# Performance work log

Hardware: AMD Instinct MI355X
Metric: run time of the kernel (lower is better)

Reference implementation:

```python
import jax, jax.numpy as jnp
import numpy as np

B, S, D = 2, 2048, 2048
H = 16
HD = D // H

def setup_inputs() -> dict:
    key = jax.random.key(0)
    ks = jax.random.split(key, 6)
    s = 1.0 / np.sqrt(D)
    return {
        "inputs": jax.random.normal(ks[0], (B, S, D), dtype=jnp.float32),
        "w_q": jax.random.normal(ks[1], (D, D), dtype=jnp.float32) * s,
        "w_k": jax.random.normal(ks[2], (D, D), dtype=jnp.float32) * s,
        "w_v": jax.random.normal(ks[3], (D, D), dtype=jnp.float32) * s,
        "w_o": jax.random.normal(ks[4], (D, D), dtype=jnp.float32) * s,
        "b_o": jax.random.normal(ks[5], (D,), dtype=jnp.float32) * 0.02,
    }

def reference(inputs, w_q, w_k, w_v, w_o, b_o):
    b, t, _ = inputs.shape
    # Linear layers: y = x @ W^T (weights stored torch-style [out, in])
    q = (inputs @ w_q.T).reshape(b, t, H, HD)
    k = (inputs @ w_k.T).reshape(b, t, H, HD)
    v = (inputs @ w_v.T).reshape(b, t, H, HD)
    # scores: [b, h, t, t]
    scores = jnp.einsum('bqhd,bkhd->bhqk', q, k)
    causal = jnp.triu(jnp.ones((t, t), dtype=bool), k=1)
    scores = jnp.where(causal, -jnp.inf, scores)
    # NOTE: source scales by sqrt(token_num) (keys.shape[2] after transpose), not sqrt(head_dim)
    scale = jnp.float32(t) ** 0.5
    attn = jax.nn.softmax(scores / scale, axis=-1)
    ctx = jnp.einsum('bhqk,bkhd->bqhd', attn, v).reshape(b, t, D)
    return ctx @ w_o.T + b_o
```

## Files before the change

kernel.cpp:

```cpp
#include <hip/hip_runtime.h>


typedef __attribute__((ext_vector_type(8))) short short8;
typedef __attribute__((ext_vector_type(4))) float f32x4;

#define SEQ 2048
#define DM  2048
#define NHD 128
#define QSCALE (0.022097086912079608f * 1.4426950408889634f)

#define EXP2F(x) __builtin_amdgcn_exp2f(x)

__device__ __forceinline__ unsigned short f2bf(float f) {
  unsigned u = __builtin_bit_cast(unsigned, f);
  u += 0x7FFFu + ((u >> 16) & 1u);
  return (unsigned short)(u >> 16);
}

__device__ __forceinline__ void gll16(const void* g, void* l) {
  __builtin_amdgcn_global_load_lds((const __attribute__((address_space(1))) void*)g,
                                   (__attribute__((address_space(3))) void*)l, 16, 0, 0);
}

template <int CTRL>
__device__ __forceinline__ float dpp_mv(float x) {
  int xi = __builtin_bit_cast(int, x);
  return __builtin_bit_cast(float,
      __builtin_amdgcn_update_dpp(xi, xi, CTRL, 0xF, 0xF, false));
}
__device__ __forceinline__ float red16_max(float x) {
  x = fmaxf(x, dpp_mv<0xB1>(x));
  x = fmaxf(x, dpp_mv<0x4E>(x));
  x = fmaxf(x, dpp_mv<0x124>(x));
  x = fmaxf(x, dpp_mv<0x128>(x));
  return x;
}
__device__ __forceinline__ float red16_sum(float x) {
  x += dpp_mv<0xB1>(x);
  x += dpp_mv<0x4E>(x);
  x += dpp_mv<0x124>(x);
  x += dpp_mv<0x128>(x);
  return x;
}

__global__ __launch_bounds__(256) void cast_bf16_k(const float* __restrict__ in,
                                                   unsigned short* __restrict__ out,
                                                   int n8) {
  int i = blockIdx.x * 256 + threadIdx.x;
  if (i >= n8) return;
  const f32x4* p = (const f32x4*)in + (size_t)i * 2;
  f32x4 a = p[0], b = p[1];
  short8 o;
  o[0] = (short)f2bf(a[0]); o[1] = (short)f2bf(a[1]);
  o[2] = (short)f2bf(a[2]); o[3] = (short)f2bf(a[3]);
  o[4] = (short)f2bf(b[0]); o[5] = (short)f2bf(b[1]);
  o[6] = (short)f2bf(b[2]); o[7] = (short)f2bf(b[3]);
  *(short8*)(out + (size_t)i * 8) = o;
}

__global__ __launch_bounds__(256) void cast_w4_k(const float* __restrict__ Wq,
                                                 const float* __restrict__ Wk,
                                                 const float* __restrict__ Wv,
                                                 const float* __restrict__ Wo,
                                                 unsigned short* __restrict__ Wqb,
                                                 unsigned short* __restrict__ Wkb,
                                                 unsigned short* __restrict__ Wvb,
                                                 unsigned short* __restrict__ Wob) {
  int i = blockIdx.x * 256 + threadIdx.x;
  int r = i >> 19, j = i & 524287;
  const float* src = (r == 0) ? Wq : (r == 1) ? Wk : (r == 2) ? Wv : Wo;
  unsigned short* dst = (r == 0) ? Wqb : (r == 1) ? Wkb : (r == 2) ? Wvb : Wob;
  float sc = (r == 0) ? QSCALE : 1.0f;
  const f32x4* p = (const f32x4*)src + (size_t)j * 2;
  f32x4 a = p[0], b = p[1];
  short8 o;
  o[0] = (short)f2bf(a[0] * sc); o[1] = (short)f2bf(a[1] * sc);
  o[2] = (short)f2bf(a[2] * sc); o[3] = (short)f2bf(a[3] * sc);
  o[4] = (short)f2bf(b[0] * sc); o[5] = (short)f2bf(b[1] * sc);
  o[6] = (short)f2bf(b[2] * sc); o[7] = (short)f2bf(b[3] * sc);
  *(short8*)(dst + (size_t)j * 8) = o;
}

__device__ __forceinline__ void gemm_core(const unsigned short* __restrict__ A,
                                          const unsigned short* __restrict__ W,
                                          unsigned short* la, unsigned short* lb,
                                          f32x4 acc[4][4],
                                          int m0, int n0) {
  const int t = threadIdx.x, w = t >> 6, l = t & 63;
  const int lr = l & 15, kb = l >> 4;
  const int wm = w >> 1, wn = w & 1;
  const int i0 = w * 64 + l, i1 = 256 + w * 64 + l;
  for (int kt = 0; kt < DM / 32; ++kt) {
    const int k0 = kt * 32;
    gll16(A + (size_t)(m0 + (i0 >> 2)) * DM + k0 + (i0 & 3) * 8, &la[(size_t)w * 512]);
    gll16(A + (size_t)(m0 + (i1 >> 2)) * DM + k0 + (i1 & 3) * 8, &la[(size_t)(4 + w) * 512]);
    gll16(W + (size_t)(n0 + (i0 >> 2)) * DM + k0 + (i0 & 3) * 8, &lb[(size_t)w * 512]);
    gll16(W + (size_t)(n0 + (i1 >> 2)) * DM + k0 + (i1 & 3) * 8, &lb[(size_t)(4 + w) * 512]);
    __syncthreads();
    short8 af[4], bfr[4];
#pragma unroll
    for (int mi = 0; mi < 4; ++mi)
      af[mi] = *(const short8*)&la[(wm * 64 + mi * 16 + lr) * 32 + kb * 8];
#pragma unroll
    for (int ni = 0; ni < 4; ++ni)
      bfr[ni] = *(const short8*)&lb[(wn * 64 + ni * 16 + lr) * 32 + kb * 8];
#pragma unroll
    for (int mi = 0; mi < 4; ++mi)
#pragma unroll
      for (int ni = 0; ni < 4; ++ni)
        acc[mi][ni] = __builtin_amdgcn_mfma_f32_16x16x32_bf16(af[mi], bfr[ni], acc[mi][ni], 0, 0, 0);
    __syncthreads();
  }
}

__global__ __launch_bounds__(256) void gemm_qk_k(const unsigned short* __restrict__ X,
                                                 const unsigned short* __restrict__ Wq,
                                                 const unsigned short* __restrict__ Wk,
                                                 unsigned short* __restrict__ Qo,
                                                 unsigned short* __restrict__ Ko) {
  __shared__ unsigned short la[128 * 32];
  __shared__ unsigned short lb[128 * 32];
  const int z = blockIdx.z;
  const unsigned short* W = z ? Wk : Wq;
  unsigned short* Y = z ? Ko : Qo;
  const int m0 = blockIdx.y * 128, n0 = blockIdx.x * 128;
  const int t = threadIdx.x, w = t >> 6, l = t & 63;
  const int lr = l & 15, kb = l >> 4;
  const int wm = w >> 1, wn = w & 1;
  f32x4 acc[4][4] = {};
  gemm_core(X, W, la, lb, acc, m0, n0);
#pragma unroll
  for (int mi = 0; mi < 4; ++mi)
#pragma unroll
    for (int ni = 0; ni < 4; ++ni)
#pragma unroll
      for (int r = 0; r < 4; ++r) {
        int row = m0 + wm * 64 + mi * 16 + kb * 4 + r;
        int col = n0 + wn * 64 + ni * 16 + lr;
        Y[(size_t)row * DM + col] = f2bf(acc[mi][ni][r]);
      }
}

__global__ __launch_bounds__(256) void gemm_vt_k(const unsigned short* __restrict__ Wv,
                                                 const unsigned short* __restrict__ X,
                                                 unsigned short* __restrict__ Vt) {
  __shared__ unsigned short la[128 * 32];
  __shared__ unsigned short lb[128 * 32];
  const int m0 = blockIdx.y * 128, n0 = blockIdx.x * 128;
  const int t = threadIdx.x, w = t >> 6, l = t & 63;
  const int lr = l & 15, kb = l >> 4;
  const int wm = w >> 1, wn = w & 1;
  f32x4 acc[4][4] = {};
  gemm_core(Wv, X, la, lb, acc, m0, n0);
#pragma unroll
  for (int mi = 0; mi < 4; ++mi)
#pragma unroll
    for (int ni = 0; ni < 4; ++ni)
#pragma unroll
      for (int r = 0; r < 4; ++r) {
        int i = m0 + wm * 64 + mi * 16 + kb * 4 + r;
        int j = n0 + wn * 64 + ni * 16 + lr;
        Vt[((size_t)(j >> 11) * 2048 + i) * 2048 + (j & 2047)] = f2bf(acc[mi][ni][r]);
      }
}

__global__ __launch_bounds__(256) void gemm_o_k(const unsigned short* __restrict__ A,
                                                const unsigned short* __restrict__ W,
                                                const float* __restrict__ bias,
                                                float* __restrict__ Y) {
  __shared__ unsigned short la[128 * 32];
  __shared__ unsigned short lb[128 * 32];
  const int m0 = blockIdx.y * 128, n0 = blockIdx.x * 128;
  const int t = threadIdx.x, w = t >> 6, l = t & 63;
  const int lr = l & 15, kb = l >> 4;
  const int wm = w >> 1, wn = w & 1;
  f32x4 acc[4][4] = {};
  gemm_core(A, W, la, lb, acc, m0, n0);
#pragma unroll
  for (int mi = 0; mi < 4; ++mi)
#pragma unroll
    for (int ni = 0; ni < 4; ++ni)
#pragma unroll
      for (int r = 0; r < 4; ++r) {
        int row = m0 + wm * 64 + mi * 16 + kb * 4 + r;
        int col = n0 + wn * 64 + ni * 16 + lr;
        Y[(size_t)row * DM + col] = acc[mi][ni][r] + bias[col];
      }
}

__device__ __forceinline__ void stage_tiles(const unsigned short* __restrict__ Kh,
                                            const unsigned short* __restrict__ Vh,
                                            unsigned short* KL, unsigned short* VL,
                                            int kv0, int t) {
#pragma unroll
  for (int c = 0; c < 4; ++c) {
    int S = c * 256 + t;
    int row = S >> 4, g = (S & 15) ^ (row & 7);
    gll16(Kh + (size_t)(kv0 + row) * DM + g * 8, KL + (size_t)S * 8);
  }
#pragma unroll
  for (int c = 0; c < 4; ++c) {
    int S = c * 256 + t;
    int d = S >> 3, g = (S & 7) ^ (d & 7);
    gll16(Vh + (size_t)d * SEQ + kv0 + g * 8, VL + (size_t)S * 8);
  }
}

__global__ __launch_bounds__(256) void attn_k(const unsigned short* __restrict__ Q,
                                              const unsigned short* __restrict__ K,
                                              const unsigned short* __restrict__ Vt,
                                              unsigned short* __restrict__ O) {
  __shared__ unsigned short KL[2][64 * 128];
  __shared__ unsigned short VL[2][128 * 64];
  __shared__ unsigned short Pb[4][16 * 64];
  const int t = threadIdx.x, w = t >> 6, l = t & 63;
  const int lr = l & 15, kb = l >> 4;
  const int id = blockIdx.x;
  const int xcd = id & 7, slot = id >> 3;
  const int bh = xcd * 4 + (slot & 3);
  const int xpair = slot >> 2;
  const int b = bh >> 4, h = bh & 15;
  const unsigned short* Kh = K + (size_t)b * SEQ * DM + h * NHD;
  const unsigned short* Vh = Vt + (size_t)bh * NHD * SEQ;

#pragma unroll 1
  for (int phase = 0; phase < 2; ++phase) {
    const int xq = phase ? (31 - xpair) : xpair;
    const int q0 = xq * 64;
    const int qw = q0 + w * 16;
    const int nkt = xq + 1;

    short8 qf[4];
    {
      const unsigned short* qp = Q + (size_t)(b * SEQ + qw + lr) * DM + h * NHD + kb * 8;
#pragma unroll
      for (int ks = 0; ks < 4; ++ks) qf[ks] = *(const short8*)(qp + ks * 32);
    }
    f32x4 ctx[8] = {};
    float mrow[4], lrow[4];
#pragma unroll
    for (int r = 0; r < 4; ++r) { mrow[r] = -3.0e4f; lrow[r] = 0.f; }

    stage_tiles(Kh, Vh, KL[0], VL[0], 0, t);
    __syncthreads();

    int cbuf = 0;
#pragma unroll 1
    for (int kt = 0; kt < nkt; ++kt) {
      const int kv0 = kt * 64;
      if (kt + 1 < nkt) stage_tiles(Kh, Vh, KL[cbuf ^ 1], VL[cbuf ^ 1], kv0 + 64, t);
      const unsigned short* Kc = KL[cbuf];
      const unsigned short* Vc = VL[cbuf];
      f32x4 s[4];
#pragma unroll
      for (int ct = 0; ct < 4; ++ct) {
        s[ct] = (f32x4){0.f, 0.f, 0.f, 0.f};
        int krow = ct * 16 + lr;
#pragma unroll
        for (int ks = 0; ks < 4; ++ks) {
          short8 bf = *(const short8*)&Kc[krow * 128 + (((ks * 4 + kb) ^ (krow & 7)) * 8)];
          s[ct] = __builtin_amdgcn_mfma_f32_16x16x32_bf16(qf[ks], bf, s[ct], 0, 0, 0);
        }
      }
      const bool needmask = (kv0 + 63 > qw);
      float pe[4][4];
#pragma unroll
      for (int r = 0; r < 4; ++r) {
        const int qi = qw + kb * 4 + r;
        float mx = -3.0e4f;
#pragma unroll
        for (int ct = 0; ct < 4; ++ct) {
          float v = s[ct][r];
          if (needmask && (kv0 + ct * 16 + lr > qi)) v = -3.0e4f;
          s[ct][r] = v;
          mx = fmaxf(mx, v);
        }
        mx = red16_max(mx);
        if (mx > mrow[r] + 8.f) {
          float alpha = EXP2F(mrow[r] - mx);
          mrow[r] = mx;
          lrow[r] *= alpha;
#pragma unroll
          for (int cc = 0; cc < 8; ++cc) ctx[cc][r] *= alpha;
        }
        float rs = 0.f;
#pragma unroll
        for (int ct = 0; ct < 4; ++ct) {
          float e = EXP2F(s[ct][r] - mrow[r]);
          pe[ct][r] = e;
          rs += e;
        }
        lrow[r] += red16_sum(rs);
      }
#pragma unroll
      for (int ct = 0; ct < 4; ++ct)
#pragma unroll
        for (int r = 0; r < 4; ++r) {
          int prow = kb * 4 + r, pcol = ct * 16 + lr;
          Pb[w][prow * 64 + (pcol ^ ((prow & 7) * 8))] = f2bf(pe[ct][r]);
        }
      short8 pa[2];
#pragma unroll
      for (int ks = 0; ks < 2; ++ks)
        pa[ks] = *(const short8*)&Pb[w][lr * 64 + (((ks * 4 + kb) ^ (lr & 7)) * 8)];
#pragma unroll
      for (int cc = 0; cc < 8; ++cc) {
        int vrow = cc * 16 + lr;
#pragma unroll
        for (int ks = 0; ks < 2; ++ks) {
          short8 vb = *(const short8*)&Vc[vrow * 64 + (((ks * 4 + kb) ^ (vrow & 7)) * 8)];
          ctx[cc] = __builtin_amdgcn_mfma_f32_16x16x32_bf16(pa[ks], vb, ctx[cc], 0, 0, 0);
        }
      }
      __syncthreads();
      cbuf ^= 1;
    }
#pragma unroll
    for (int r = 0; r < 4; ++r) {
      float inv = 1.f / lrow[r];
      size_t rowoff = (size_t)(b * SEQ + qw + kb * 4 + r) * DM + h * NHD;
#pragma unroll
      for (int cc = 0; cc < 8; ++cc)
        O[rowoff + cc * 16 + lr] = f2bf(ctx[cc][r] * inv);
    }
  }
}

extern "C" void kernel_launch(void* const* d_in, const int* in_sizes, int n_in,
                              void* d_out, int out_size, void* d_ws, size_t ws_size,
                              hipStream_t stream) {
  const float* X  = (const float*)d_in[0];
  const float* Wq = (const float*)d_in[1];
  const float* Wk = (const float*)d_in[2];
  const float* Wv = (const float*)d_in[3];
  const float* Wo = (const float*)d_in[4];
  const float* bo = (const float*)d_in[5];
  float* out = (float*)d_out;

  unsigned short* ws = (unsigned short*)d_ws;
  unsigned short* Xb  = ws;
  unsigned short* Wqb = ws + 8388608;
  unsigned short* Wkb = ws + 12582912;
  unsigned short* Wvb = ws + 16777216;
  unsigned short* Wob = ws + 20971520;
  unsigned short* Qb  = ws + 25165824;
  unsigned short* Kb  = ws + 33554432;
  unsigned short* Vtb = ws + 41943040;
  unsigned short* Cb  = ws + 50331648;

  cast_bf16_k<<<4096, 256, 0, stream>>>(X, Xb, 1048576);
  cast_w4_k<<<8192, 256, 0, stream>>>(Wq, Wk, Wv, Wo, Wqb, Wkb, Wvb, Wob);

  gemm_qk_k<<<dim3(16, 32, 2), 256, 0, stream>>>(Xb, Wqb, Wkb, Qb, Kb);
  gemm_vt_k<<<dim3(32, 16), 256, 0, stream>>>(Wvb, Xb, Vtb);
  attn_k<<<512, 256, 0, stream>>>(Qb, Kb, Vtb, Cb);
  gemm_o_k<<<dim3(16, 32), 256, 0, stream>>>(Cb, Wob, bo, out);
}
```

Baseline: 291.9 us.

## Pipeline GEMM k-loop with 4-stage LDS ring and XOR-swizzled layout

The shared GEMM core now prefetches three k-tiles ahead into a four-buffer LDS ring using direct global-to-LDS loads. It waits on vmcnt counts plus a single barrier per iteration instead of two full syncthreads, so loads overlap MFMA work. An XOR swizzle on the 16-byte chunk index is applied both when staging and when reading fragments, meant to reduce LDS bank conflicts. LDS use per block grows fourfold, which can lower occupancy.

```diff
diff --git a/kernel.cpp b/kernel.cpp
--- a/kernel.cpp
+++ b/kernel.cpp
@@ -81,6 +81,20 @@
   *(short8*)(dst + (size_t)j * 8) = o;
 }
 
+#define WAITV(N) asm volatile("s_waitcnt vmcnt(" #N ")" ::: "memory")
+
+__device__ __forceinline__ void stage_op(const unsigned short* __restrict__ base,
+                                         int m0, int k0,
+                                         unsigned short* lbuf, int t) {
+#pragma unroll
+  for (int c = 0; c < 2; ++c) {
+    int S = c * 256 + t;
+    int row = S >> 2, g = S & 3;
+    int gs = g ^ ((row >> 1) & 3);
+    gll16(base + (size_t)(m0 + row) * DM + k0 + gs * 8, lbuf + (size_t)S * 8);
+  }
+}
+
 __device__ __forceinline__ void gemm_core(const unsigned short* __restrict__ A,
                                           const unsigned short* __restrict__ W,
                                           unsigned short* la, unsigned short* lb,
@@ -89,27 +103,39 @@
   const int t = threadIdx.x, w = t >> 6, l = t & 63;
   const int lr = l & 15, kb = l >> 4;
   const int wm = w >> 1, wn = w & 1;
-  const int i0 = w * 64 + l, i1 = 256 + w * 64 + l;
-  for (int kt = 0; kt < DM / 32; ++kt) {
-    const int k0 = kt * 32;
-    gll16(A + (size_t)(m0 + (i0 >> 2)) * DM + k0 + (i0 & 3) * 8, &la[(size_t)w * 512]);
-    gll16(A + (size_t)(m0 + (i1 >> 2)) * DM + k0 + (i1 & 3) * 8, &la[(size_t)(4 + w) * 512]);
-    gll16(W + (size_t)(n0 + (i0 >> 2)) * DM + k0 + (i0 & 3) * 8, &lb[(size_t)w * 512]);
-    gll16(W + (size_t)(n0 + (i1 >> 2)) * DM + k0 + (i1 & 3) * 8, &lb[(size_t)(4 + w) * 512]);
-    __syncthreads();
+  stage_op(A, m0, 0, la, t);          stage_op(W, n0, 0, lb, t);
+  stage_op(A, m0, 32, la + 4096, t);  stage_op(W, n0, 32, lb + 4096, t);
+  stage_op(A, m0, 64, la + 8192, t);  stage_op(W, n0, 64, lb + 8192, t);
+
+#pragma unroll 4
+  for (int kt = 0; kt < 64; ++kt) {
+    if (kt <= 61) { WAITV(8); }
+    else if (kt == 62) { WAITV(4); }
+    else { WAITV(0); }
+    __builtin_amdgcn_s_barrier();
+    if (kt + 3 < 64) {
+      int buf = (kt + 3) & 3;
+      stage_op(A, m0, (kt + 3) * 32, la + buf * 4096, t);
+      stage_op(W, n0, (kt + 3) * 32, lb + buf * 4096, t);
+    }
+    const unsigned short* lA = la + (kt & 3) * 4096;
+    const unsigned short* lB = lb + (kt & 3) * 4096;
     short8 af[4], bfr[4];
 #pragma unroll
-    for (int mi = 0; mi < 4; ++mi)
-      af[mi] = *(const short8*)&la[(wm * 64 + mi * 16 + lr) * 32 + kb * 8];
-#pragma unroll
-    for (int ni = 0; ni < 4; ++ni)
-      bfr[ni] = *(const short8*)&lb[(wn * 64 + ni * 16 + lr) * 32 + kb * 8];
+    for (int mi = 0; mi < 4; ++mi) {
+      int row = wm * 64 + mi * 16 + lr;
+      af[mi] = *(const short8*)&lA[row * 32 + ((kb ^ ((row >> 1) & 3)) * 8)];
+    }
+#pragma unroll
+    for (int ni = 0; ni < 4; ++ni) {
+      int row = wn * 64 + ni * 16 + lr;
+      bfr[ni] = *(const short8*)&lB[row * 32 + ((kb ^ ((row >> 1) & 3)) * 8)];
+    }
 #pragma unroll
     for (int mi = 0; mi < 4; ++mi)
 #pragma unroll
       for (int ni = 0; ni < 4; ++ni)
         acc[mi][ni] = __builtin_amdgcn_mfma_f32_16x16x32_bf16(af[mi], bfr[ni], acc[mi][ni], 0, 0, 0);
-    __syncthreads();
   }
 }
 
@@ -118,8 +144,8 @@
                                                  const unsigned short* __restrict__ Wk,
                                                  unsigned short* __restrict__ Qo,
                                                  unsigned short* __restrict__ Ko) {
-  __shared__ unsigned short la[128 * 32];
-  __shared__ unsigned short lb[128 * 32];
+  __shared__ unsigned short la[4 * 4096];
+  __shared__ unsigned short lb[4 * 4096];
   const int z = blockIdx.z;
   const unsigned short* W = z ? Wk : Wq;
   unsigned short* Y = z ? Ko : Qo;
@@ -144,8 +170,8 @@
 __global__ __launch_bounds__(256) void gemm_vt_k(const unsigned short* __restrict__ Wv,
                                                  const unsigned short* __restrict__ X,
                                                  unsigned short* __restrict__ Vt) {
-  __shared__ unsigned short la[128 * 32];
-  __shared__ unsigned short lb[128 * 32];
+  __shared__ unsigned short la[4 * 4096];
+  __shared__ unsigned short lb[4 * 4096];
   const int m0 = blockIdx.y * 128, n0 = blockIdx.x * 128;
   const int t = threadIdx.x, w = t >> 6, l = t & 63;
   const int lr = l & 15, kb = l >> 4;
@@ -168,8 +194,8 @@
                                                 const unsigned short* __restrict__ W,
                                                 const float* __restrict__ bias,
                                                 float* __restrict__ Y) {
-  __shared__ unsigned short la[128 * 32];
-  __shared__ unsigned short lb[128 * 32];
+  __shared__ unsigned short la[4 * 4096];
+  __shared__ unsigned short lb[4 * 4096];
   const int m0 = blockIdx.y * 128, n0 = blockIdx.x * 128;
   const int t = threadIdx.x, w = t >> 6, l = t & 63;
   const int lr = l & 15, kb = l >> 4;
```

Result: slower. 307.0 us (+5.2%).

## Rewrite projection GEMMs as 256x256 double-buffered pipelined tiles with swizzled LDS

Applied to the files above, without the earlier changes.

Replaces the 128x128, K=32, single-buffered GEMM core with a 256x256 tile using 512 threads, K=64 steps, and double-buffered LDS. Loads are issued directly to LDS, with XOR swizzle to avoid bank conflicts. Each K step runs in four quadrant phases that interleave staging of the next tile with MFMA compute, using explicit vmcnt waits, raw barriers and setprio. The aim is to raise arithmetic intensity and hide global-load latency in the Q/K/V/O projections. The cost is 128KB of LDS per block and larger register use, and the grids get fewer blocks (128-256), which can underfill the CUs.

```diff
diff --git a/kernel.cpp b/kernel.cpp
--- a/kernel.cpp
+++ b/kernel.cpp
@@ -7,9 +7,11 @@
 #define SEQ 2048
 #define DM  2048
 #define NHD 128
+#define NT  32
 #define QSCALE (0.022097086912079608f * 1.4426950408889634f)
 
 #define EXP2F(x) __builtin_amdgcn_exp2f(x)
+#define WAITV(N) asm volatile("s_waitcnt vmcnt(" #N ")" ::: "memory")
 
 __device__ __forceinline__ unsigned short f2bf(float f) {
   unsigned u = __builtin_bit_cast(unsigned, f);
@@ -81,111 +83,167 @@
   *(short8*)(dst + (size_t)j * 8) = o;
 }
 
-__device__ __forceinline__ void gemm_core(const unsigned short* __restrict__ A,
-                                          const unsigned short* __restrict__ W,
-                                          unsigned short* la, unsigned short* lb,
-                                          f32x4 acc[4][4],
-                                          int m0, int n0) {
-  const int t = threadIdx.x, w = t >> 6, l = t & 63;
+__device__ __forceinline__ void stage_half(const unsigned short* __restrict__ gbase,
+                                           unsigned short* lhalf, int tid) {
+#pragma unroll
+  for (int c = 0; c < 2; ++c) {
+    int G = c * 512 + tid;
+    int row = G >> 3, g = G & 7;
+    int gs = g ^ (row & 7);
+    gll16(gbase + (size_t)row * DM + gs * 8, lhalf + (size_t)G * 8);
+  }
+}
+
+#define PHASE(MH, NH, STG, WV)                                                  \
+  {                                                                             \
+    const unsigned short* lAh = lA + (MH) * 8192;                               \
+    const unsigned short* lBh = lB + (NH) * 8192;                               \
+    short8 af[4][2], bfr[2][2];                                                 \
+    _Pragma("unroll") for (int mi = 0; mi < 4; ++mi)                            \
+      _Pragma("unroll") for (int ks = 0; ks < 2; ++ks) {                        \
+        int row = wm * 64 + mi * 16 + lr;                                       \
+        af[mi][ks] = *(const short8*)&lAh[row * 64 + (((ks * 4 + kb) ^ (row & 7)) * 8)]; \
+      }                                                                         \
+    _Pragma("unroll") for (int ni = 0; ni < 2; ++ni)                            \
+      _Pragma("unroll") for (int ks = 0; ks < 2; ++ks) {                        \
+        int row = wn * 32 + ni * 16 + lr;                                       \
+        bfr[ni][ks] = *(const short8*)&lBh[row * 64 + (((ks * 4 + kb) ^ (row & 7)) * 8)]; \
+      }                                                                         \
+    STG;                                                                        \
+    __builtin_amdgcn_s_barrier();                                               \
+    __builtin_amdgcn_s_setprio(1);                                              \
+    _Pragma("unroll") for (int mi = 0; mi < 4; ++mi)                            \
+      _Pragma("unroll") for (int ni = 0; ni < 2; ++ni) {                        \
+        acc[MH][NH][mi][ni] = __builtin_amdgcn_mfma_f32_16x16x32_bf16(          \
+            af[mi][0], bfr[ni][0], acc[MH][NH][mi][ni], 0, 0, 0);               \
+        acc[MH][NH][mi][ni] = __builtin_amdgcn_mfma_f32_16x16x32_bf16(          \
+            af[mi][1], bfr[ni][1], acc[MH][NH][mi][ni], 0, 0, 0);               \
+      }                                                                         \
+    __builtin_amdgcn_s_setprio(0);                                              \
+    WV;                                                                         \
+    __builtin_amdgcn_s_barrier();                                               \
+  }
+
+__device__ __forceinline__ void gemm256_core(const unsigned short* __restrict__ A,
+                                             const unsigned short* __restrict__ B,
+                                             unsigned short* LA, unsigned short* LB,
+                                             f32x4 acc[2][2][4][2], int m0, int n0) {
+  const int tid = threadIdx.x;
+  const int w = tid >> 6, l = tid & 63;
   const int lr = l & 15, kb = l >> 4;
-  const int wm = w >> 1, wn = w & 1;
-  const int i0 = w * 64 + l, i1 = 256 + w * 64 + l;
-  for (int kt = 0; kt < DM / 32; ++kt) {
-    const int k0 = kt * 32;
-    gll16(A + (size_t)(m0 + (i0 >> 2)) * DM + k0 + (i0 & 3) * 8, &la[(size_t)w * 512]);
-    gll16(A + (size_t)(m0 + (i1 >> 2)) * DM + k0 + (i1 & 3) * 8, &la[(size_t)(4 + w) * 512]);
-    gll16(W + (size_t)(n0 + (i0 >> 2)) * DM + k0 + (i0 & 3) * 8, &lb[(size_t)w * 512]);
-    gll16(W + (size_t)(n0 + (i1 >> 2)) * DM + k0 + (i1 & 3) * 8, &lb[(size_t)(4 + w) * 512]);
-    __syncthreads();
-    short8 af[4], bfr[4];
-#pragma unroll
-    for (int mi = 0; mi < 4; ++mi)
-      af[mi] = *(const short8*)&la[(wm * 64 + mi * 16 + lr) * 32 + kb * 8];
-#pragma unroll
-    for (int ni = 0; ni < 4; ++ni)
-      bfr[ni] = *(const short8*)&lb[(wn * 64 + ni * 16 + lr) * 32 + kb * 8];
-#pragma unroll
-    for (int mi = 0; mi < 4; ++mi)
-#pragma unroll
-      for (int ni = 0; ni < 4; ++ni)
-        acc[mi][ni] = __builtin_amdgcn_mfma_f32_16x16x32_bf16(af[mi], bfr[ni], acc[mi][ni], 0, 0, 0);
-    __syncthreads();
-  }
-}
-
-__global__ __launch_bounds__(256) void gemm_qk_k(const unsigned short* __restrict__ X,
-                                                 const unsigned short* __restrict__ Wq,
-                                                 const unsigned short* __restrict__ Wk,
-                                                 unsigned short* __restrict__ Qo,
-                                                 unsigned short* __restrict__ Ko) {
-  __shared__ unsigned short la[128 * 32];
-  __shared__ unsigned short lb[128 * 32];
+  const int wm = w >> 2, wn = w & 3;
+
+  stage_half(A + (size_t)m0 * DM, LA, tid);
+  stage_half(B + (size_t)n0 * DM, LB, tid);
+  stage_half(B + (size_t)n0 * DM + (size_t)128 * DM, LB + 8192, tid);
+  stage_half(A + (size_t)m0 * DM + (size_t)128 * DM, LA + 8192, tid);
+  WAITV(4);
+  __builtin_amdgcn_s_barrier();
+
+#pragma unroll 1
+  for (int t = 0; t < NT; ++t) {
+    const unsigned short* lA = LA + (t & 1) * 16384;
+    const unsigned short* lB = LB + (t & 1) * 16384;
+    unsigned short* sA = LA + ((t + 1) & 1) * 16384;
+    unsigned short* sB = LB + ((t + 1) & 1) * 16384;
+    const unsigned short* gA = A + (size_t)m0 * DM + (t + 1) * 64;
+    const unsigned short* gB = B + (size_t)n0 * DM + (t + 1) * 64;
+    const bool st = (t + 1 < NT);
+    PHASE(0, 0, if (st) stage_half(gA, sA, tid),
+                if (st) { WAITV(4); } else { WAITV(2); });
+    PHASE(0, 1, if (st) stage_half(gB, sB, tid),
+                if (st) { WAITV(4); } else { WAITV(0); });
+    PHASE(1, 0, if (st) stage_half(gB + (size_t)128 * DM, sB + 8192, tid), );
+    PHASE(1, 1, if (st) stage_half(gA + (size_t)128 * DM, sA + 8192, tid),
+                if (st) { WAITV(4); });
+  }
+}
+
+__global__ __launch_bounds__(512, 2) void gemm_qk_k(const unsigned short* __restrict__ X,
+                                                    const unsigned short* __restrict__ Wq,
+                                                    const unsigned short* __restrict__ Wk,
+                                                    unsigned short* __restrict__ Qo,
+                                                    unsigned short* __restrict__ Ko) {
+  __shared__ unsigned short LA[32768];
+  __shared__ unsigned short LB[32768];
   const int z = blockIdx.z;
   const unsigned short* W = z ? Wk : Wq;
   unsigned short* Y = z ? Ko : Qo;
-  const int m0 = blockIdx.y * 128, n0 = blockIdx.x * 128;
-  const int t = threadIdx.x, w = t >> 6, l = t & 63;
+  const int m0 = blockIdx.y * 256, n0 = blockIdx.x * 256;
+  const int tid = threadIdx.x, w = tid >> 6, l = tid & 63;
   const int lr = l & 15, kb = l >> 4;
-  const int wm = w >> 1, wn = w & 1;
-  f32x4 acc[4][4] = {};
-  gemm_core(X, W, la, lb, acc, m0, n0);
-#pragma unroll
-  for (int mi = 0; mi < 4; ++mi)
-#pragma unroll
-    for (int ni = 0; ni < 4; ++ni)
-#pragma unroll
-      for (int r = 0; r < 4; ++r) {
-        int row = m0 + wm * 64 + mi * 16 + kb * 4 + r;
-        int col = n0 + wn * 64 + ni * 16 + lr;
-        Y[(size_t)row * DM + col] = f2bf(acc[mi][ni][r]);
-      }
-}
-
-__global__ __launch_bounds__(256) void gemm_vt_k(const unsigned short* __restrict__ Wv,
-                                                 const unsigned short* __restrict__ X,
-                                                 unsigned short* __restrict__ Vt) {
-  __shared__ unsigned short la[128 * 32];
-  __shared__ unsigned short lb[128 * 32];
-  const int m0 = blockIdx.y * 128, n0 = blockIdx.x * 128;
-  const int t = threadIdx.x, w = t >> 6, l = t & 63;
+  const int wm = w >> 2, wn = w & 3;
+  f32x4 acc[2][2][4][2] = {};
+  gemm256_core(X, W, LA, LB, acc, m0, n0);
+#pragma unroll
+  for (int mh = 0; mh < 2; ++mh)
+#pragma unroll
+    for (int nh = 0; nh < 2; ++nh)
+#pragma unroll
+      for (int mi = 0; mi < 4; ++mi)
+#pragma unroll
+        for (int ni = 0; ni < 2; ++ni)
+#pragma unroll
+          for (int rr = 0; rr < 4; ++rr) {
+            int row = m0 + mh * 128 + wm * 64 + mi * 16 + kb * 4 + rr;
+            int col = n0 + nh * 128 + wn * 32 + ni * 16 + lr;
+            Y[(size_t)row * DM + col] = f2bf(acc[mh][nh][mi][ni][rr]);
+          }
+}
+
+__global__ __launch_bounds__(512, 2) void gemm_vt_k(const unsigned short* __restrict__ Wv,
+                                                    const unsigned short* __restrict__ X,
+                                                    unsigned short* __restrict__ Vt) {
+  __shared__ unsigned short LA[32768];
+  __shared__ unsigned short LB[32768];
+  const int m0 = blockIdx.y * 256, n0 = blockIdx.x * 256;
+  const int tid = threadIdx.x, w = tid >> 6, l = tid & 63;
   const int lr = l & 15, kb = l >> 4;
-  const int wm = w >> 1, wn = w & 1;
-  f32x4 acc[4][4] = {};
-  gemm_core(Wv, X, la, lb, acc, m0, n0);
-#pragma unroll
-  for (int mi = 0; mi < 4; ++mi)
-#pragma unroll
-    for (int ni = 0; ni < 4; ++ni)
-#pragma unroll
-      for (int r = 0; r < 4; ++r) {
-        int i = m0 + wm * 64 + mi * 16 + kb * 4 + r;
-        int j = n0 + wn * 64 + ni * 16 + lr;
-        Vt[((size_t)(j >> 11) * 2048 + i) * 2048 + (j & 2047)] = f2bf(acc[mi][ni][r]);
-      }
-}
-
-__global__ __launch_bounds__(256) void gemm_o_k(const unsigned short* __restrict__ A,
-                                                const unsigned short* __restrict__ W,
-                                                const float* __restrict__ bias,
-                                                float* __restrict__ Y) {
-  __shared__ unsigned short la[128 * 32];
-  __shared__ unsigned short lb[128 * 32];
-  const int m0 = blockIdx.y * 128, n0 = blockIdx.x * 128;
-  const int t = threadIdx.x, w = t >> 6, l = t & 63;
+  const int wm = w >> 2, wn = w & 3;
+  f32x4 acc[2][2][4][2] = {};
+  gemm256_core(Wv, X, LA, LB, acc, m0, n0);
+#pragma unroll
+  for (int mh = 0; mh < 2; ++mh)
+#pragma unroll
+    for (int nh = 0; nh < 2; ++nh)
+#pragma unroll
+      for (int mi = 0; mi < 4; ++mi)
+#pragma unroll
+        for (int ni = 0; ni < 2; ++ni)
+#pragma unroll
+          for (int rr = 0; rr < 4; ++rr) {
+            int i = m0 + mh * 128 + wm * 64 + mi * 16 + kb * 4 + rr;
+            int j = n0 + nh * 128 + wn * 32 + ni * 16 + lr;
+            Vt[((size_t)(j >> 11) * 2048 + i) * 2048 + (j & 2047)] = f2bf(acc[mh][nh][mi][ni][rr]);
+          }
+}
+
+__global__ __launch_bounds__(512, 2) void gemm_o_k(const unsigned short* __restrict__ A,
+                                                   const unsigned short* __restrict__ W,
+                                                   const float* __restrict__ bias,
+                                                   float* __restrict__ Y) {
+  __shared__ unsigned short LA[32768];
+  __shared__ unsigned short LB[32768];
+  const int m0 = blockIdx.y * 256, n0 = blockIdx.x * 256;
+  const int tid = threadIdx.x, w = tid >> 6, l = tid & 63;
   const int lr = l & 15, kb = l >> 4;
-  const int wm = w >> 1, wn = w & 1;
-  f32x4 acc[4][4] = {};
-  gemm_core(A, W, la, lb, acc, m0, n0);
-#pragma unroll
-  for (int mi = 0; mi < 4; ++mi)
-#pragma unroll
-    for (int ni = 0; ni < 4; ++ni)
-#pragma unroll
-      for (int r = 0; r < 4; ++r) {
-        int row = m0 + wm * 64 + mi * 16 + kb * 4 + r;
-        int col = n0 + wn * 64 + ni * 16 + lr;
-        Y[(size_t)row * DM + col] = acc[mi][ni][r] + bias[col];
-      }
+  const int wm = w >> 2, wn = w & 3;
+  f32x4 acc[2][2][4][2] = {};
+  gemm256_core(A, W, LA, LB, acc, m0, n0);
+#pragma unroll
+  for (int mh = 0; mh < 2; ++mh)
+#pragma unroll
+    for (int nh = 0; nh < 2; ++nh)
+#pragma unroll
+      for (int mi = 0; mi < 4; ++mi)
+#pragma unroll
+        for (int ni = 0; ni < 2; ++ni)
+#pragma unroll
+          for (int rr = 0; rr < 4; ++rr) {
+            int row = m0 + mh * 128 + wm * 64 + mi * 16 + kb * 4 + rr;
+            int col = n0 + nh * 128 + wn * 32 + ni * 16 + lr;
+            Y[(size_t)row * DM + col] = acc[mh][nh][mi][ni][rr] + bias[col];
+          }
 }
 
 __device__ __forceinline__ void stage_tiles(const unsigned short* __restrict__ Kh,
@@ -351,8 +409,8 @@
   cast_bf16_k<<<4096, 256, 0, stream>>>(X, Xb, 1048576);
   cast_w4_k<<<8192, 256, 0, stream>>>(Wq, Wk, Wv, Wo, Wqb, Wkb, Wvb, Wob);
 
-  gemm_qk_k<<<dim3(16, 32, 2), 256, 0, stream>>>(Xb, Wqb, Wkb, Qb, Kb);
-  gemm_vt_k<<<dim3(32, 16), 256, 0, stream>>>(Wvb, Xb, Vtb);
+  gemm_qk_k<<<dim3(8, 16, 2), 512, 0, stream>>>(Xb, Wqb, Wkb, Qb, Kb);
+  gemm_vt_k<<<dim3(16, 8), 512, 0, stream>>>(Wvb, Xb, Vtb);
   attn_k<<<512, 256, 0, stream>>>(Qb, Kb, Vtb, Cb);
-  gemm_o_k<<<dim3(16, 32), 256, 0, stream>>>(Cb, Wob, bo, out);
-}
+  gemm_o_k<<<dim3(8, 16), 512, 0, stream>>>(Cb, Wob, bo, out);
+}
```

New measurement: 307.3 us. 1.05x slower.
